# Performance work log

Hardware: AMD Instinct MI355X
Metric: run time of the kernel (lower is better)

The kernel has to match this reference:

```python
import jax, jax.numpy as jnp
import numpy as np

HEADS, HEAD_SIZE, FREQS, MAX_PERIOD = 16, 64, 256, 10000
D_MODEL = 1024
NEG_INF = -1e9


def sinusoid_embedding(seq_len, frequencies, max_period):
    # Interleaved sin/cos sinusoid table, shape (seq_len, frequencies).
    pos = np.arange(seq_len, dtype=np.float64)[:, None]
    idx = np.arange(frequencies)[None, :]
    inv_freq = max_period ** (-(idx // 2 * 2) / frequencies)
    angle = pos * inv_freq
    table = np.where(idx % 2 == 0, np.sin(angle), np.cos(angle))
    return table.astype(np.float32)


def relative_causal(scores):
    # scores: (b, n, q, v) with v indexing relative distance d = q - k.
    # Returns a[..., q, k] = scores[..., q, q - k] (k > q entries are masked later).
    L = scores.shape[-1]
    d = jnp.clip(jnp.arange(L)[:, None] - jnp.arange(L)[None, :], 0, L - 1)  # (q, k)
    return jnp.take_along_axis(scores, d[None, None, :, :], axis=-1)


def setup_inputs() -> dict:
    key = jax.random.key(0)
    ks = jax.random.split(key, 4)
    u = np.sqrt(3.0)
    inp = jax.random.normal(ks[0], (2, 2048, D_MODEL), dtype=jnp.float32)
    qkv = jax.random.uniform(ks[1], (D_MODEL, 3, HEADS, HEAD_SIZE), jnp.float32, -u, u)
    q_bias = jnp.zeros((HEADS, HEAD_SIZE), jnp.float32)
    positional = jax.random.uniform(ks[2], (FREQS, HEADS, HEAD_SIZE), jnp.float32, -u, u)
    out_kernel = jax.random.uniform(ks[3], (HEADS * HEAD_SIZE, D_MODEL), jnp.float32, -u, u)
    out_bias = jnp.zeros((D_MODEL,), jnp.float32)
    return {"input": inp, "qkv": qkv, "q_bias": q_bias, "positional": positional,
            "out_kernel": out_kernel, "out_bias": out_bias}


def reference(input, qkv, q_bias, positional, out_kernel, out_bias):
    b, s, x = input.shape
    n, h = HEADS, HEAD_SIZE
    # QKV projection with unit-scaling forward factor.
    w = qkv * (3.0 * x * h * n) ** -0.25
    q, k, v = jnp.einsum('bsx,xAnh->Abnsh', input, w)  # each (b, n, s, h)
    q = q + q_bias[:, None, :]
    # Content scores.
    a = jnp.einsum('bnqh,bnkh->bnqk', q, k) * h ** -0.5
    # Relative-positional scores (Transformer-XL style).
    sins = jnp.asarray(np.sqrt(2.0) * sinusoid_embedding(s, FREQS, MAX_PERIOD))
    emb = jnp.einsum('sf,fnh->nsh', sins, positional * FREQS ** -0.5)
    pos_scores = jnp.einsum('bnqh,nvh->bnqv', q, emb) * h ** -0.5
    a = a + relative_causal(pos_scores)
    # Causal mask + softmax.
    mask = jnp.tril(jnp.ones((s, s), dtype=bool))
    a = jax.nn.softmax(jnp.where(mask, a, NEG_INF), axis=-1)
    # Weighted sum and output projection (Dense, scale_for='both').
    o = jnp.einsum('bnqk,bnkh->bqnh', a, v).reshape(b, s, n * h)
    fan_in, fan_out = out_kernel.shape
    out = o @ (out_kernel * (fan_in * fan_out) ** -0.25) + out_bias
    return out
```

## Files before the change

kernel.cpp:

```cpp
#include <hip/hip_runtime.h>
#include <math.h>

#define BATCH 2
#define SEQ 2048
#define DMODEL 1024
#define HEADS 16
#define HSIZE 64
#define FREQS 256
#define NH 1024
#define QKVN 3072

typedef __bf16 bf16;
typedef __bf16 bf16x8 __attribute__((ext_vector_type(8)));
typedef float f32x4 __attribute__((ext_vector_type(4)));

static __device__ __forceinline__ unsigned short bf16_bits(float v) {
    bf16 b = (bf16)v; return __builtin_bit_cast(unsigned short, b);
}

static __device__ __forceinline__ void gload16(const void* g, void* l) {
    __builtin_amdgcn_global_load_lds(
        (const __attribute__((address_space(1))) unsigned int*)g,
        (__attribute__((address_space(3))) unsigned int*)l, 16, 0, 0);
}

__global__ __launch_bounds__(256) void prep_kernel(
    const float* __restrict__ inp, const float* __restrict__ qkv_w,
    const float* __restrict__ out_kernel, const float* __restrict__ positional,
    bf16* __restrict__ a_bf, bf16* __restrict__ wt_qkv,
    bf16* __restrict__ wt_out, bf16* __restrict__ wt_pos,
    bf16* __restrict__ sins_bf)
{
    __shared__ float tile[32][33];
    const int id = blockIdx.x, t = threadIdx.x;

    if (id < 4096) {
        int i = id * 256 + t;
        float4 v = ((const float4*)inp)[i];
        ushort4 o;
        o.x = bf16_bits(v.x); o.y = bf16_bits(v.y);
        o.z = bf16_bits(v.z); o.w = bf16_bits(v.w);
        ((ushort4*)a_bf)[i] = o;
        return;
    }
    if (id < 6144) {
        int i = (id - 4096) * 256 + t;
        int s = i >> 8, f = i & 255;
        double e = -(double)((f >> 1) << 1) / (double)FREQS;
        double invf = pow(10000.0, e);
        double ang = (double)s * invf;
        double v = (f & 1) ? cos(ang) : sin(ang);
        sins_bf[i] = (bf16)(float)(1.4142135623730951 * v);
        return;
    }
    int id2 = id - 6144;
    const float* src; bf16* dst; int R, C, c0, r0;
    if (id2 < 3072) {
        src = qkv_w; dst = wt_qkv; R = 1024; C = 3072;
        c0 = (id2 % 96) * 32; r0 = (id2 / 96) * 32;
    } else if (id2 < 4096) {
        id2 -= 3072;
        src = out_kernel; dst = wt_out; R = 1024; C = 1024;
        c0 = (id2 & 31) * 32; r0 = (id2 >> 5) * 32;
    } else {
        id2 -= 4096;
        src = positional; dst = wt_pos; R = 256; C = 1024;
        c0 = (id2 & 31) * 32; r0 = (id2 >> 5) * 32;
    }
    const int tx = t & 31, ty = t >> 5;
#pragma unroll
    for (int i = 0; i < 4; i++)
        tile[ty + i * 8][tx] = src[(size_t)(r0 + ty + i * 8) * C + c0 + tx];
    __syncthreads();
#pragma unroll
    for (int i = 0; i < 4; i++)
        dst[(size_t)(c0 + ty + i * 8) * R + r0 + tx] = (bf16)tile[tx][ty + i * 8];
}

__global__ __launch_bounds__(256) void mfma_gemm_out(
    const bf16* __restrict__ A, const bf16* __restrict__ Bt,
    int K, float alpha, const float* __restrict__ bias,
    float* __restrict__ outf)
{
    __shared__ __align__(16) bf16 Atile[2][64 * 32];
    __shared__ __align__(16) bf16 Btile[2][128 * 32];

    const int t    = threadIdx.x;
    const int lane = t & 63;
    const int w    = t >> 6;
    const int quad = lane >> 4;
    const int l16  = lane & 15;

    const int m0 = blockIdx.y * 64, n0 = blockIdx.x * 128;

    const int rS = t >> 2;
    const int cS = (t & 3) ^ ((rS >> 1) & 3);
    const bf16* ag0 = A  + (size_t)(m0 + rS) * K + cS * 8;
    const bf16* bg0 = Bt + (size_t)(n0 + rS) * K + cS * 8;
    const bf16* bg1 = bg0 + (size_t)64 * K;

    int aoff[4], boff[2];
#pragma unroll
    for (int mi = 0; mi < 4; ++mi) {
        int r = mi * 16 + l16;
        aoff[mi] = r * 32 + ((quad ^ ((r >> 1) & 3)) * 8);
    }
#pragma unroll
    for (int ni = 0; ni < 2; ++ni) {
        int r = w * 32 + ni * 16 + l16;
        boff[ni] = r * 32 + ((quad ^ ((r >> 1) & 3)) * 8);
    }

    gload16(ag0, (char*)Atile[0] + t * 16);
    gload16(bg0, (char*)Btile[0] + t * 16);
    gload16(bg1, (char*)Btile[0] + 4096 + t * 16);

    const int nK = K >> 5;
    f32x4 acc[4][2] = {};

    for (int kk = 0; kk < nK; ++kk) {
        __syncthreads();
        if (kk + 1 < nK) {
            ag0 += 32; bg0 += 32; bg1 += 32;
            char* ad = (char*)Atile[(kk + 1) & 1];
            char* bd = (char*)Btile[(kk + 1) & 1];
            gload16(ag0, ad + t * 16);
            gload16(bg0, bd + t * 16);
            gload16(bg1, bd + 4096 + t * 16);
        }
        const bf16* ab = Atile[kk & 1];
        const bf16* bb = Btile[kk & 1];
        bf16x8 af[4], bfr[2];
#pragma unroll
        for (int mi = 0; mi < 4; ++mi) af[mi] = *(const bf16x8*)(ab + aoff[mi]);
#pragma unroll
        for (int ni = 0; ni < 2; ++ni) bfr[ni] = *(const bf16x8*)(bb + boff[ni]);
#pragma unroll
        for (int mi = 0; mi < 4; ++mi)
#pragma unroll
            for (int ni = 0; ni < 2; ++ni)
                acc[mi][ni] = __builtin_amdgcn_mfma_f32_16x16x32_bf16(
                    af[mi], bfr[ni], acc[mi][ni], 0, 0, 0);
    }

#pragma unroll
    for (int mi = 0; mi < 4; ++mi)
#pragma unroll
        for (int ni = 0; ni < 2; ++ni) {
            int col = n0 + w * 32 + ni * 16 + l16;
            float bb = bias[col];
#pragma unroll
            for (int rg = 0; rg < 4; ++rg) {
                int row = m0 + mi * 16 + quad * 4 + rg;
                outf[(size_t)row * NH + col] = acc[mi][ni][rg] * alpha + bb;
            }
        }
}

__global__ __launch_bounds__(512) void mfma_gemm_qkv(
    const bf16* __restrict__ A, const bf16* __restrict__ Bt,
    float alpha, const float* __restrict__ bias,
    bf16* __restrict__ ob0, bf16* __restrict__ ob1, bf16* __restrict__ ob2,
    const bf16* __restrict__ A2, const bf16* __restrict__ Bt2,
    bf16* __restrict__ ob3, float alpha2)
{
    __shared__ __align__(16) bf16 Atile[2][256 * 32];
    __shared__ __align__(16) bf16 Btile[2][128 * 32];

    const int t    = threadIdx.x;
    const int lane = t & 63;
    const int w    = t >> 6;
    const int quad = lane >> 4;
    const int l16  = lane & 15;
    const int wm   = (w >> 1) * 64;
    const int wn   = (w & 1) * 64;

    bool embp = false;
    int m0 = blockIdx.y * 256, n0 = blockIdx.x * 128, Kl = DMODEL;
    const bf16* Ap = A; const bf16* Btp = Bt; float al = alpha;
    if (blockIdx.x >= 24) {
        if (blockIdx.y >= 8) return;
        embp = true;
        n0 = (blockIdx.x - 24) * 128;
        Kl = FREQS; Ap = A2; Btp = Bt2; al = alpha2;
    }
    const bool swapv = !embp && (n0 >= 2048);

    const int rS = t >> 2;
    const int cS = (t & 3) ^ ((rS >> 1) & 3);
    const bf16* ag0 = Ap  + (size_t)(m0 + rS) * Kl + cS * 8;
    const bf16* ag1 = ag0 + (size_t)128 * Kl;
    const bf16* bg0 = Btp + (size_t)(n0 + rS) * Kl + cS * 8;

    int aoff[4], boff[4];
#pragma unroll
    for (int mi = 0; mi < 4; ++mi) {
        int r = wm + mi * 16 + l16;
        aoff[mi] = r * 32 + ((quad ^ ((r >> 1) & 3)) * 8);
    }
#pragma unroll
    for (int ni = 0; ni < 4; ++ni) {
        int r = wn + ni * 16 + l16;
        boff[ni] = r * 32 + ((quad ^ ((r >> 1) & 3)) * 8);
    }

    gload16(ag0, (char*)Atile[0] + t * 16);
    gload16(ag1, (char*)Atile[0] + 8192 + t * 16);
    gload16(bg0, (char*)Btile[0] + t * 16);

    const int nK = Kl >> 5;
    f32x4 acc[4][4] = {};

    for (int kk = 0; kk < nK; ++kk) {
        __syncthreads();
        if (kk + 1 < nK) {
            ag0 += 32; ag1 += 32; bg0 += 32;
            char* ad = (char*)Atile[(kk + 1) & 1];
            char* bd = (char*)Btile[(kk + 1) & 1];
            gload16(ag0, ad + t * 16);
            gload16(ag1, ad + 8192 + t * 16);
            gload16(bg0, bd + t * 16);
        }
        const bf16* ab = Atile[kk & 1];
        const bf16* bb = Btile[kk & 1];
        bf16x8 af[4], bfr[4];
#pragma unroll
        for (int mi = 0; mi < 4; ++mi) af[mi] = *(const bf16x8*)(ab + aoff[mi]);
#pragma unroll
        for (int ni = 0; ni < 4; ++ni) bfr[ni] = *(const bf16x8*)(bb + boff[ni]);

        if (!swapv) {
#pragma unroll
            for (int mi = 0; mi < 4; ++mi)
#pragma unroll
                for (int ni = 0; ni < 4; ++ni)
                    acc[mi][ni] = __builtin_amdgcn_mfma_f32_16x16x32_bf16(
                        af[mi], bfr[ni], acc[mi][ni], 0, 0, 0);
        } else {
#pragma unroll
            for (int mi = 0; mi < 4; ++mi)
#pragma unroll
                for (int ni = 0; ni < 4; ++ni)
                    acc[mi][ni] = __builtin_amdgcn_mfma_f32_16x16x32_bf16(
                        bfr[ni], af[mi], acc[mi][ni], 0, 0, 0);
        }
    }

    if (embp) {
#pragma unroll
        for (int mi = 0; mi < 4; ++mi)
#pragma unroll
            for (int ni = 0; ni < 4; ++ni) {
                int col = n0 + wn + ni * 16 + l16;
                int head = col >> 6, h = col & 63;
#pragma unroll
                for (int rg = 0; rg < 4; ++rg) {
                    int d = m0 + wm + mi * 16 + quad * 4 + rg;
                    int hs = h ^ (((d + 63) & 7) << 3);
                    ob3[((size_t)(head * SEQ + d)) * 64 + hs] =
                        (bf16)(acc[mi][ni][rg] * al);
                }
            }
    } else if (swapv) {
#pragma unroll
        for (int mi = 0; mi < 4; ++mi)
#pragma unroll
            for (int ni = 0; ni < 4; ++ni) {
                int mcol = m0 + wm + mi * 16 + l16;
                int bb = mcol >> 11, s = mcol & 2047;
#pragma unroll
                for (int rg = 0; rg < 4; ++rg) {
                    int hg = n0 + wn + ni * 16 + quad * 4 + rg;
                    int head = (hg & 1023) >> 6, h = hg & 63;
                    int ss = s ^ ((h & 7) << 3);
                    ob2[((size_t)((bb * 16 + head) * 64 + h)) * SEQ + ss] =
                        (bf16)(acc[mi][ni][rg] * al);
                }
            }
    } else {
        const int whichk = (n0 >= 1024);
#pragma unroll
        for (int mi = 0; mi < 4; ++mi)
#pragma unroll
            for (int ni = 0; ni < 4; ++ni) {
                int cg   = (n0 + wn + ni * 16 + l16) & 1023;
                int head = cg >> 6, h = cg & 63;
                float qbv = whichk ? 0.0f : bias[cg];
#pragma unroll
                for (int rg = 0; rg < 4; ++rg) {
                    int row = m0 + wm + mi * 16 + quad * 4 + rg;
                    int bb = row >> 11, s = row & 2047;
                    float v = acc[mi][ni][rg] * al;
                    if (whichk) {
                        int hs = h ^ ((s & 7) << 3);
                        ob1[((size_t)((bb * 16 + head) * SEQ + s)) * 64 + hs] = (bf16)v;
                    } else {
                        ob0[((size_t)((bb * 16 + head) * SEQ + s)) * 64 + h] =
                            (bf16)((v + qbv) * 0.125f);
                    }
                }
            }
    }
}

__device__ const unsigned char YQC[24]  = {15,15,7,14,14,13,13,6,12,12,11,11,
                                           5,10,10,9,9,4,8,8,3,2,1,0};
__device__ const unsigned char YPRT[24] = {0,1,2,0,1,0,1,2,0,1,0,1,
                                           2,0,1,0,1,2,0,1,2,2,2,2};

__global__ __launch_bounds__(256, 2) void attn_kernel(
    const bf16* __restrict__ Qb, const bf16* __restrict__ Kb,
    const bf16* __restrict__ Vtb, const bf16* __restrict__ Eb,
    bf16* __restrict__ o, float* __restrict__ Opart, float* __restrict__ Lpart)
{
    __shared__ __align__(16) bf16 Ks[2][4096];
    __shared__ __align__(16) bf16 Vts[2][4096];
    __shared__ __align__(16) bf16 Es[256 * 64];
    __shared__ __align__(16) bf16 PS[4][16][72];

    const int t    = threadIdx.x;
    const int lane = t & 63;
    const int w    = t >> 6;
    const int quad = lane >> 4;
    const int l16  = lane & 15;

    const int bx = blockIdx.x;
    const int b  = bx >> 4, n = bx & 15;
    const int yy = blockIdx.y;
    const int qc = YQC[yy];
    const int pr = YPRT[yy];
    const int q0 = qc * 128;
    const int KT = 2 * qc + 2;
    const int kt0 = (pr == 1) ? (qc + 1) : 0;
    const int kt1 = (pr == 0) ? (qc + 1) : KT;
    const bool haspeel = (pr != 0);
    const bool split   = (pr != 2);
    const int qw0 = q0 + 16 * w;
    const int qw1 = qw0 + 64;

    const bf16* __restrict__ Qp = Qb  + (size_t)bx * SEQ * 64;
    const bf16* __restrict__ Kp = Kb  + (size_t)bx * SEQ * 64;
    const bf16* __restrict__ Vp = Vtb + (size_t)bx * SEQ * 64;
    const bf16* __restrict__ Ep = Eb  + (size_t)n  * SEQ * 64;

    const int key8 = (l16 & 7) << 3;
    const int ec0  = ((quad * 8) ^ key8) * 2;
    const int ec1  = ((32 + quad * 8) ^ key8) * 2;

    bf16x8 qf[2][2];
    qf[0][0] = *(const bf16x8*)(Qp + (size_t)(qw0 + l16) * 64 + quad * 8);
    qf[0][1] = *(const bf16x8*)(Qp + (size_t)(qw0 + l16) * 64 + 32 + quad * 8);
    qf[1][0] = *(const bf16x8*)(Qp + (size_t)(qw1 + l16) * 64 + quad * 8);
    qf[1][1] = *(const bf16x8*)(Qp + (size_t)(qw1 + l16) * 64 + 32 + quad * 8);

    int dsta[4];
    bool condp[4];
#pragma unroll
    for (int rg = 0; rg < 4; ++rg) {
        int rr   = quad * 4 + rg;
        int l16c = (rr + 15 - l16) & 15;
        dsta[rg]  = ((lane & 48) + l16c) << 2;
        condp[rg] = rr > l16c;
    }

    f32x4 O[2][4] = {};
    float lsum[2][4] = {};

    {
        const bf16* ksrc = Kp + kt0 * 4096;
        char* kd = (char*)Ks[kt0 & 1];
        char* vd = (char*)Vts[kt0 & 1];
        gload16(ksrc + t * 8,        kd + t * 16);
        gload16(ksrc + 2048 + t * 8, kd + 4096 + t * 16);
        gload16(Vp + (size_t)(t >> 3) * SEQ + kt0 * 64 + (t & 7) * 8,        vd + t * 16);
        gload16(Vp + (size_t)((t >> 3) + 32) * SEQ + kt0 * 64 + (t & 7) * 8, vd + 4096 + t * 16);
        const long D0 = (long)q0 - 64 * kt0 - 63;
        const int rI0 = (-64 * kt0) & 255;
#pragma unroll
        for (int g = 0; g < 6; ++g) {
            const int sI = (rI0 + 32 * g) & 255;
            gload16(Ep + (D0 + 32 * g) * 64 + t * 8, (char*)Es + sI * 128 + t * 16);
        }
    }

    auto load_kv = [&](const char* kb, const char* vb,
                       bf16x8 (&kf)[4][2], bf16x8 (&vf)[4][2]) {
#pragma unroll
        for (int j = 0; j < 4; ++j) {
            const char* kp = kb + (j * 16 + l16) * 128;
            kf[j][0] = *(const bf16x8*)(kp + ec0);
            kf[j][1] = *(const bf16x8*)(kp + ec1);
            const char* vp = vb + (j * 16 + l16) * 128;
            vf[j][0] = *(const bf16x8*)(vp + ec0);
            vf[j][1] = *(const bf16x8*)(vp + ec1);
        }
    };
    auto eread = [&](int rb, bf16x8 (&ef)[5][2]) {
#pragma unroll
        for (int jj = 0; jj < 5; ++jj) {
            const char* ep = (const char*)Es + ((rb + 16 * jj + l16) & 255) * 128;
            ef[jj][0] = *(const bf16x8*)(ep + ec0);
            ef[jj][1] = *(const bf16x8*)(ep + ec1);
        }
    };
    auto qkmfma = [&](const bf16x8 (&q2)[2], const bf16x8 (&kf)[4][2],
                      f32x4 (&S)[4]) {
#pragma unroll
        for (int j = 0; j < 4; ++j) {
            f32x4 a = {0, 0, 0, 0};
            a = __builtin_amdgcn_mfma_f32_16x16x32_bf16(q2[1], kf[j][1], a, 0, 0, 0);
            a = __builtin_amdgcn_mfma_f32_16x16x32_bf16(q2[0], kf[j][0], a, 0, 0, 0);
            S[j] = a;
        }
    };
    auto pamfma = [&](const bf16x8 (&q2)[2], const bf16x8 (&ef)[5][2],
                      f32x4 (&pa)[5]) {
#pragma unroll
        for (int jj = 0; jj < 5; ++jj) {
            f32x4 a = {0, 0, 0, 0};
            a = __builtin_amdgcn_mfma_f32_16x16x32_bf16(q2[1], ef[jj][1], a, 0, 0, 0);
            a = __builtin_amdgcn_mfma_f32_16x16x32_bf16(q2[0], ef[jj][0], a, 0, 0, 0);
            pa[jj] = a;
        }
    };
    auto smax = [&](int kq, f32x4 (&S)[4], const f32x4 (&pa)[5], float (&ls)[4]) {
#pragma unroll
        for (int j = 0; j < 4; ++j) {
#pragma unroll
            for (int rg = 0; rg < 4; ++rg) {
                float vsel = condp[rg] ? pa[4 - j][rg] : pa[3 - j][rg];
                int pv = __builtin_amdgcn_ds_permute(dsta[rg], __float_as_int(vsel));
                float sv = S[j][rg] + __int_as_float(pv);
                bool valid = (j * 16 + l16) <= (kq + quad * 4 + rg);
                S[j][rg] = valid ? __expf(sv) : 0.0f;
            }
        }
#pragma unroll
        for (int rg = 0; rg < 4; ++rg)
            ls[rg] += S[0][rg] + S[1][rg] + S[2][rg] + S[3][rg];
    };
    auto ps_write = [&](const f32x4 (&S)[4]) {
#pragma unroll
        for (int j = 0; j < 4; ++j)
#pragma unroll
            for (int rg = 0; rg < 4; ++rg)
                PS[w][quad * 4 + rg][j * 16 + l16] = (bf16)S[j][rg];
    };
    auto pvmfma = [&](const bf16x8 (&vf)[4][2], f32x4 (&Oc)[4]) {
        bf16x8 pf0 = *(const bf16x8*)(&PS[w][l16][quad * 8]);
        bf16x8 pf1 = *(const bf16x8*)(&PS[w][l16][32 + quad * 8]);
#pragma unroll
        for (int j4 = 0; j4 < 4; ++j4) {
            Oc[j4] = __builtin_amdgcn_mfma_f32_16x16x32_bf16(pf1, vf[j4][1], Oc[j4], 0, 0, 0);
            Oc[j4] = __builtin_amdgcn_mfma_f32_16x16x32_bf16(pf0, vf[j4][0], Oc[j4], 0, 0, 0);
        }
    };

    const int ktE = kt1 - (haspeel ? 1 : 0);
    for (int kt = kt0; kt < ktE; ++kt) {
        const int k0 = kt * 64;
        __syncthreads();

        const int nt = kt + 1;
        if (nt < kt1) {
            bf16* kd = Ks[nt & 1];
            bf16* vd = Vts[nt & 1];
            const bf16* ksrc = Kp + nt * 4096;
            gload16(ksrc + t * 8,        (char*)kd + t * 16);
            gload16(ksrc + 2048 + t * 8, (char*)kd + 4096 + t * 16);
            gload16(Vp + (size_t)(t >> 3) * SEQ + nt * 64 + (t & 7) * 8,
                    (char*)vd + t * 16);
            gload16(Vp + (size_t)((t >> 3) + 32) * SEQ + nt * 64 + (t & 7) * 8,
                    (char*)vd + 4096 + t * 16);
            const long d0 = (long)q0 - nt * 64 - 63;
            const int rI = (-64 * nt) & 255;
            gload16(Ep + d0 * 64 + t * 8,        (char*)Es + rI * 128 + t * 16);
            gload16(Ep + (d0 + 32) * 64 + t * 8, (char*)Es + rI * 128 + 4096 + t * 16);
        }

        bf16x8 kf[4][2], vf[4][2];
        load_kv((const char*)Ks[kt & 1], (const char*)Vts[kt & 1], kf, vf);

        bf16x8 ef0[5][2];
        eread(16 * w - k0, ef0);
        f32x4 S0[4], pa0[5];
        __builtin_amdgcn_s_setprio(1);
        qkmfma(qf[0], kf, S0);
        pamfma(qf[0], ef0, pa0);
        __builtin_amdgcn_s_setprio(0);
        smax(qw0 - k0, S0, pa0, lsum[0]);

        bf16x8 ef1[5][2];
        eread(16 * w + 64 - k0, ef1);
        ps_write(S0);

        f32x4 S1[4], pa1[5];
        __builtin_amdgcn_s_setprio(1);
        qkmfma(qf[1], kf, S1);
        pamfma(qf[1], ef1, pa1);
        pvmfma(vf, O[0]);
        __builtin_amdgcn_s_setprio(0);

        smax(qw1 - k0, S1, pa1, lsum[1]);
        ps_write(S1);
        __builtin_amdgcn_s_setprio(1);
        pvmfma(vf, O[1]);
        __builtin_amdgcn_s_setprio(0);
    }

    if (haspeel) {
        const int kt = kt1 - 1, k0 = kt * 64;
        __syncthreads();
        bf16x8 kf[4][2], vf[4][2];
        load_kv((const char*)Ks[kt & 1], (const char*)Vts[kt & 1], kf, vf);
        bf16x8 ef1[5][2];
        eread(16 * w + 64 - k0, ef1);
        f32x4 S1[4], pa1[5];
        qkmfma(qf[1], kf, S1);
        pamfma(qf[1], ef1, pa1);
        smax(qw1 - k0, S1, pa1, lsum[1]);
        ps_write(S1);
        pvmfma(vf, O[1]);
    }

    if (!split) {
#pragma unroll
        for (int c = 0; c < 2; ++c) {
#pragma unroll
            for (int rg = 0; rg < 4; ++rg) {
                float s = lsum[c][rg];
                s += __shfl_xor(s, 1);
                s += __shfl_xor(s, 2);
                s += __shfl_xor(s, 4);
                s += __shfl_xor(s, 8);
                float inv = 1.0f / s;
                int q = (c ? qw1 : qw0) + quad * 4 + rg;
                size_t ro = ((size_t)(b * SEQ + q)) * NH + n * 64;
                o[ro +  0 + l16] = (bf16)(O[c][0][rg] * inv);
                o[ro + 16 + l16] = (bf16)(O[c][1][rg] * inv);
                o[ro + 32 + l16] = (bf16)(O[c][2][rg] * inv);
                o[ro + 48 + l16] = (bf16)(O[c][3][rg] * inv);
            }
        }
    } else {
        const int pslot = pr;
        float* Ob = Opart + ((size_t)(pslot * 32 + bx)) * 1024 * 64;
        float* Lb = Lpart + ((size_t)(pslot * 32 + bx)) * 1024;
#pragma unroll
        for (int c = 0; c < 2; ++c) {
#pragma unroll
            for (int rg = 0; rg < 4; ++rg) {
                float s = lsum[c][rg];
                s += __shfl_xor(s, 1);
                s += __shfl_xor(s, 2);
                s += __shfl_xor(s, 4);
                s += __shfl_xor(s, 8);
                int q = (c ? qw1 : qw0) + quad * 4 + rg;
                int rloc = q - 1024;
                size_t ro = (size_t)rloc * 64;
                Ob[ro +  0 + l16] = O[c][0][rg];
                Ob[ro + 16 + l16] = O[c][1][rg];
                Ob[ro + 32 + l16] = O[c][2][rg];
                Ob[ro + 48 + l16] = O[c][3][rg];
                if (l16 == 0) Lb[rloc] = s;
            }
        }
    }
}

__global__ __launch_bounds__(256) void merge_kernel(
    const float* __restrict__ Opart, const float* __restrict__ Lpart,
    bf16* __restrict__ o)
{
    int idx = blockIdx.x * 256 + threadIdx.x;
    int h4 = idx & 15;
    int r  = (idx >> 4) & 1023;
    int bx = idx >> 14;
    size_t i0 = (((size_t)bx        * 1024 + r) * 64 + h4 * 4);
    size_t i1 = (((size_t)(32 + bx) * 1024 + r) * 64 + h4 * 4);
    float4 a = *(const float4*)(Opart + i0);
    float4 c = *(const float4*)(Opart + i1);
    float inv = 1.0f / (Lpart[bx * 1024 + r] + Lpart[32 * 1024 + bx * 1024 + r]);
    int b = bx >> 4, n = bx & 15;
    size_t ro = ((size_t)(b * SEQ + 1024 + r)) * NH + n * 64 + h4 * 4;
    ushort4 wv;
    wv.x = bf16_bits((a.x + c.x) * inv);
    wv.y = bf16_bits((a.y + c.y) * inv);
    wv.z = bf16_bits((a.z + c.z) * inv);
    wv.w = bf16_bits((a.w + c.w) * inv);
    *(ushort4*)(o + ro) = wv;
}

extern "C" void kernel_launch(void* const* d_in, const int* in_sizes, int n_in,
                              void* d_out, int out_size, void* d_ws, size_t ws_size,
                              hipStream_t stream) {
    const float* inp        = (const float*)d_in[0];
    const float* qkv_w      = (const float*)d_in[1];
    const float* q_bias     = (const float*)d_in[2];
    const float* positional = (const float*)d_in[3];
    const float* out_kernel = (const float*)d_in[4];
    const float* out_bias   = (const float*)d_in[5];

    char* p = (char*)d_ws;
    auto alloc = [&](size_t bytes) {
        char* q = p; p += (bytes + 255) & ~(size_t)255; return q;
    };
    bf16* qbuf    = (bf16*)alloc((size_t)BATCH * HEADS * SEQ * HSIZE * 2);
    bf16* kbuf    = (bf16*)alloc((size_t)BATCH * HEADS * SEQ * HSIZE * 2);
    bf16* vtbuf   = (bf16*)alloc((size_t)BATCH * HEADS * SEQ * HSIZE * 2);
    bf16* embT    = (bf16*)alloc((size_t)HEADS * SEQ * HSIZE * 2);
    bf16* sins_bf = (bf16*)alloc((size_t)SEQ * FREQS * 2);
    bf16* obuf    = (bf16*)alloc((size_t)BATCH * SEQ * NH * 2);
    bf16* wt_out  = (bf16*)alloc((size_t)NH * DMODEL * 2);
    bf16* wt_pos  = (bf16*)alloc((size_t)NH * FREQS * 2);
    bf16* a_bf    = (bf16*)alloc((size_t)BATCH * SEQ * DMODEL * 2);
    bf16* wt_qkv  = (bf16*)alloc((size_t)QKVN * DMODEL * 2);
    (void)       alloc((size_t)2097152);
    float* Opart  = (float*)a_bf;
    float* Lpart  = (float*)wt_pos;

    const float qkv_scale = (float)pow(3.0 * DMODEL * HSIZE * HEADS, -0.25);
    const float emb_scale = 0.0625f;
    const float out_scale = 0.03125f;

    prep_kernel<<<10496, 256, 0, stream>>>(
        inp, qkv_w, out_kernel, positional, a_bf, wt_qkv, wt_out, wt_pos, sins_bf);

    mfma_gemm_qkv<<<dim3(32, 16), 512, 0, stream>>>(
        a_bf, wt_qkv, qkv_scale, q_bias, qbuf, kbuf, vtbuf,
        sins_bf, wt_pos, embT, emb_scale);

    attn_kernel<<<dim3(32, 24), 256, 0, stream>>>(
        qbuf, kbuf, vtbuf, embT, obuf, Opart, Lpart);

    merge_kernel<<<2048, 256, 0, stream>>>(Opart, Lpart, obuf);

    mfma_gemm_out<<<dim3(8, 64), 256, 0, stream>>>(
        obuf, wt_out, DMODEL, out_scale, out_bias, (float*)d_out);
}
```

Before: 256.5 us.

## Fuse split-KV merge into attention kernel via atomic ticket counters

Drops the separate merge kernel launch. Each split attention block now bumps an atomic ticket per (batch-head, query chunk) after writing its partial O and L, and the second block to arrive does the merge and writes the bf16 output. The ticket array is zeroed by an extra block in the prep kernel. This saves one launch and a global round trip, at the cost of threadfences, an atomic per block, and the merge work now sitting on the tail of the last-finishing attention blocks.

```diff
diff --git a/kernel.cpp b/kernel.cpp
--- a/kernel.cpp
+++ b/kernel.cpp
@@ -29,11 +29,15 @@
     const float* __restrict__ out_kernel, const float* __restrict__ positional,
     bf16* __restrict__ a_bf, bf16* __restrict__ wt_qkv,
     bf16* __restrict__ wt_out, bf16* __restrict__ wt_pos,
-    bf16* __restrict__ sins_bf)
+    bf16* __restrict__ sins_bf, int* __restrict__ tickets)
 {
     __shared__ float tile[32][33];
     const int id = blockIdx.x, t = threadIdx.x;
 
+    if (id == 10496) {
+        tickets[t & 255] = 0;
+        return;
+    }
     if (id < 4096) {
         int i = id * 256 + t;
         float4 v = ((const float4*)inp)[i];
@@ -311,12 +315,14 @@
 __global__ __launch_bounds__(256, 2) void attn_kernel(
     const bf16* __restrict__ Qb, const bf16* __restrict__ Kb,
     const bf16* __restrict__ Vtb, const bf16* __restrict__ Eb,
-    bf16* __restrict__ o, float* __restrict__ Opart, float* __restrict__ Lpart)
+    bf16* __restrict__ o, float* __restrict__ Opart, float* __restrict__ Lpart,
+    int* __restrict__ tickets)
 {
     __shared__ __align__(16) bf16 Ks[2][4096];
     __shared__ __align__(16) bf16 Vts[2][4096];
     __shared__ __align__(16) bf16 Es[256 * 64];
     __shared__ __align__(16) bf16 PS[4][16][72];
+    __shared__ int mflag;
 
     const int t    = threadIdx.x;
     const int lane = t & 63;
@@ -565,30 +571,38 @@
                 if (l16 == 0) Lb[rloc] = s;
             }
         }
-    }
-}
-
-__global__ __launch_bounds__(256) void merge_kernel(
-    const float* __restrict__ Opart, const float* __restrict__ Lpart,
-    bf16* __restrict__ o)
-{
-    int idx = blockIdx.x * 256 + threadIdx.x;
-    int h4 = idx & 15;
-    int r  = (idx >> 4) & 1023;
-    int bx = idx >> 14;
-    size_t i0 = (((size_t)bx        * 1024 + r) * 64 + h4 * 4);
-    size_t i1 = (((size_t)(32 + bx) * 1024 + r) * 64 + h4 * 4);
-    float4 a = *(const float4*)(Opart + i0);
-    float4 c = *(const float4*)(Opart + i1);
-    float inv = 1.0f / (Lpart[bx * 1024 + r] + Lpart[32 * 1024 + bx * 1024 + r]);
-    int b = bx >> 4, n = bx & 15;
-    size_t ro = ((size_t)(b * SEQ + 1024 + r)) * NH + n * 64 + h4 * 4;
-    ushort4 wv;
-    wv.x = bf16_bits((a.x + c.x) * inv);
-    wv.y = bf16_bits((a.y + c.y) * inv);
-    wv.z = bf16_bits((a.z + c.z) * inv);
-    wv.w = bf16_bits((a.w + c.w) * inv);
-    *(ushort4*)(o + ro) = wv;
+
+        __threadfence();
+        __syncthreads();
+        if (t == 0)
+            mflag = (atomicAdd(&tickets[bx * 8 + (qc - 8)], 1) == 1);
+        __syncthreads();
+        if (mflag) {
+            __threadfence();
+            const int rbase = (qc - 8) * 128;
+            const float* O0 = Opart + (size_t)bx * 65536;
+            const float* O1 = Opart + (size_t)(32 + bx) * 65536;
+            const float* L0 = Lpart + bx * 1024;
+            const float* L1 = Lpart + 32 * 1024 + bx * 1024;
+#pragma unroll
+            for (int i = 0; i < 8; ++i) {
+                int idx = t * 8 + i;
+                int r   = rbase + (idx >> 4);
+                int h4  = (idx & 15) * 4;
+                size_t po = (size_t)(r - 1024 + 1024) * 0 + (size_t)r * 64 + h4;
+                float4 a = *(const float4*)(O0 + po);
+                float4 c = *(const float4*)(O1 + po);
+                float inv = 1.0f / (L0[r] + L1[r]);
+                size_t ro = ((size_t)(b * SEQ + 1024 + r)) * NH + n * 64 + h4;
+                ushort4 wv;
+                wv.x = bf16_bits((a.x + c.x) * inv);
+                wv.y = bf16_bits((a.y + c.y) * inv);
+                wv.z = bf16_bits((a.z + c.z) * inv);
+                wv.w = bf16_bits((a.w + c.w) * inv);
+                *(ushort4*)(o + ro) = wv;
+            }
+        }
+    }
 }
 
 extern "C" void kernel_launch(void* const* d_in, const int* in_sizes, int n_in,
@@ -616,6 +630,7 @@
     bf16* a_bf    = (bf16*)alloc((size_t)BATCH * SEQ * DMODEL * 2);
     bf16* wt_qkv  = (bf16*)alloc((size_t)QKVN * DMODEL * 2);
     (void)       alloc((size_t)2097152);
+    int* tickets  = (int*)alloc(1024);
     float* Opart  = (float*)a_bf;
     float* Lpart  = (float*)wt_pos;
 
@@ -623,17 +638,16 @@
     const float emb_scale = 0.0625f;
     const float out_scale = 0.03125f;
 
-    prep_kernel<<<10496, 256, 0, stream>>>(
-        inp, qkv_w, out_kernel, positional, a_bf, wt_qkv, wt_out, wt_pos, sins_bf);
+    prep_kernel<<<10497, 256, 0, stream>>>(
+        inp, qkv_w, out_kernel, positional, a_bf, wt_qkv, wt_out, wt_pos,
+        sins_bf, tickets);
 
     mfma_gemm_qkv<<<dim3(32, 16), 512, 0, stream>>>(
         a_bf, wt_qkv, qkv_scale, q_bias, qbuf, kbuf, vtbuf,
         sins_bf, wt_pos, embT, emb_scale);
 
     attn_kernel<<<dim3(32, 24), 256, 0, stream>>>(
-        qbuf, kbuf, vtbuf, embT, obuf, Opart, Lpart);
-
-    merge_kernel<<<2048, 256, 0, stream>>>(Opart, Lpart, obuf);
+        qbuf, kbuf, vtbuf, embT, obuf, Opart, Lpart, tickets);
 
     mfma_gemm_out<<<dim3(8, 64), 256, 0, stream>>>(
         obuf, wt_out, DMODEL, out_scale, out_bias, (float*)d_out);
```

After: 343.8 us. +34.0%, slower.
